# Kernel tuning notes

Measured on AMD Instinct MI355X. Metric: run time of the kernel, lower is better.

Reference implementation:

```python
import jax, jax.numpy as jnp
import numpy as np

LN_EPS = 1e-5

def _layer_norm(x, w, b):
    m = jnp.mean(x, axis=-1, keepdims=True)
    v = jnp.mean(jnp.square(x - m), axis=-1, keepdims=True)
    return (x - m) * jax.lax.rsqrt(v + LN_EPS) * w + b

def setup_inputs() -> dict:
    key = jax.random.key(0)
    ks = jax.random.split(key, 6)
    B, T, D, H = 64, 512, 512, 512
    x = jax.random.normal(ks[0], (B, T, D), dtype=jnp.float32)
    h = jax.random.normal(ks[1], (B, H), dtype=jnp.float32)
    # orthogonal-ish init approximated by scaled normal (math-equivalent shapes)
    w_ih = jax.random.normal(ks[2], (3 * H, D), dtype=jnp.float32) / np.sqrt(D)
    b_ih = jnp.zeros((3 * H,), dtype=jnp.float32)
    w_hh = jax.random.normal(ks[3], (3 * H, H), dtype=jnp.float32) / np.sqrt(H)
    b_hh = jnp.zeros((3 * H,), dtype=jnp.float32)
    ln_r_w = jnp.ones((H,), jnp.float32); ln_r_b = jnp.zeros((H,), jnp.float32)
    ln_z_w = jnp.ones((H,), jnp.float32); ln_z_b = jnp.zeros((H,), jnp.float32)
    ln_n_w = jnp.ones((H,), jnp.float32); ln_n_b = jnp.zeros((H,), jnp.float32)
    return dict(x=x, h=h, w_ih=w_ih, b_ih=b_ih, w_hh=w_hh, b_hh=b_hh,
                ln_r_w=ln_r_w, ln_r_b=ln_r_b, ln_z_w=ln_z_w, ln_z_b=ln_z_b,
                ln_n_w=ln_n_w, ln_n_b=ln_n_b)

def reference(x, h, w_ih, b_ih, w_hh, b_hh, ln_r_w, ln_r_b, ln_z_w, ln_z_b, ln_n_w, ln_n_b):
    H = h.shape[-1]
    # precompute input gate projections for all timesteps: [B, T, 3H] -> [T, B, 3H]
    x_gates_all = jnp.einsum('btd,gd->btg', x, w_ih) + b_ih
    x_gates_all = jnp.swapaxes(x_gates_all, 0, 1)

    def step(h, x_gates):
        h_gates = jnp.matmul(h, w_hh.T) + b_hh
        x_r, x_z, x_n = jnp.split(x_gates, 3, axis=-1)
        h_r, h_z, h_n = jnp.split(h_gates, 3, axis=-1)
        r = jax.nn.sigmoid(_layer_norm(x_r + h_r, ln_r_w, ln_r_b))
        z = jax.nn.sigmoid(_layer_norm(x_z + h_z, ln_z_w, ln_z_b))
        n = jnp.tanh(_layer_norm(x_n + r * h_n, ln_n_w, ln_n_b))
        h_new = (1.0 - z) * n + z * h
        return h_new, h_new

    h_last, out_tbh = jax.lax.scan(step, h, x_gates_all)
    out = jnp.swapaxes(out_tbh, 0, 1)  # [B, T, H]
    return out, h_last
```

## Files before the change

### kernel.cpp

```cpp
#include <hip/hip_runtime.h>
#include <hip/hip_bf16.h>

#define B_ 64
#define T_ 512
#define D_ 512
#define H_ 512
#define G3 1536
#define NBLK 16

typedef float f32x4 __attribute__((ext_vector_type(4)));
typedef __bf16 bf16x8 __attribute__((ext_vector_type(8)));

#define LDSP 56
#define WPITCH 520

union bfpack { bf16x8 v; __hip_bfloat16 h[8]; };

__device__ inline bf16x8 cvt8(const float* __restrict__ p) {
    float4 f0 = *(const float4*)p;
    float4 f1 = *(const float4*)(p + 4);
    bfpack u;
    u.h[0] = __float2bfloat16(f0.x); u.h[1] = __float2bfloat16(f0.y);
    u.h[2] = __float2bfloat16(f0.z); u.h[3] = __float2bfloat16(f0.w);
    u.h[4] = __float2bfloat16(f1.x); u.h[5] = __float2bfloat16(f1.y);
    u.h[6] = __float2bfloat16(f1.z); u.h[7] = __float2bfloat16(f1.w);
    return u.v;
}

__global__ void k0_init(const float* __restrict__ h_in,
                        __hip_bfloat16* __restrict__ hb,
                        unsigned int* __restrict__ ctr) {
    int i = blockIdx.x * blockDim.x + threadIdx.x;
    if (i < B_ * H_) hb[i] = __float2bfloat16(h_in[i]);
    if (i < 1024)    ctr[i] = 0u;
}

__global__ __launch_bounds__(256) void k1_xgemm(
    const float* __restrict__ X, const float* __restrict__ W,
    const float* __restrict__ bias, __hip_bfloat16* __restrict__ XG)
{
    __shared__ __align__(16) __hip_bfloat16 la[128 * LDSP];
    __shared__ __align__(16) __hip_bfloat16 lb[128 * LDSP];
    int tid = threadIdx.x, bx = blockIdx.x;
    int m0 = (bx / 12) * 128, n0 = (bx % 12) * 128;
    int wave = tid >> 6, lane = tid & 63;
    int wh = wave >> 1, ww = wave & 1;
    int l15 = lane & 15, kq = lane >> 4;

    f32x4 acc[4][4];
    #pragma unroll
    for (int i = 0; i < 4; i++)
        #pragma unroll
        for (int j = 0; j < 4; j++) acc[i][j] = (f32x4){0.f, 0.f, 0.f, 0.f};

    for (int kt = 0; kt < 16; ++kt) {
        int k0 = kt * 32;
        for (int s = tid; s < 512; s += 256) {
            int r = s >> 2, c = s & 3;
            *(bf16x8*)&la[r * LDSP + c * 8] = cvt8(&X[(size_t)(m0 + r) * D_ + k0 + c * 8]);
            *(bf16x8*)&lb[r * LDSP + c * 8] = cvt8(&W[(size_t)(n0 + r) * D_ + k0 + c * 8]);
        }
        __syncthreads();
        bf16x8 af[4], bq[4];
        #pragma unroll
        for (int i = 0; i < 4; i++)
            af[i] = *(const bf16x8*)&la[(wh * 64 + i * 16 + l15) * LDSP + kq * 8];
        #pragma unroll
        for (int j = 0; j < 4; j++)
            bq[j] = *(const bf16x8*)&lb[(ww * 64 + j * 16 + l15) * LDSP + kq * 8];
        #pragma unroll
        for (int i = 0; i < 4; i++)
            #pragma unroll
            for (int j = 0; j < 4; j++)
                acc[i][j] = __builtin_amdgcn_mfma_f32_16x16x32_bf16(af[i], bq[j], acc[i][j], 0, 0, 0);
        __syncthreads();
    }
    #pragma unroll
    for (int i = 0; i < 4; i++)
        #pragma unroll
        for (int j = 0; j < 4; j++)
            #pragma unroll
            for (int r = 0; r < 4; r++) {
                int m = m0 + wh * 64 + i * 16 + kq * 4 + r;
                int n = n0 + ww * 64 + j * 16 + l15;
                int b = m >> 9, t = m & 511;
                XG[((size_t)t * B_ + b) * G3 + n] = __float2bfloat16(acc[i][j][r] + bias[n]);
            }
}

__global__ __launch_bounds__(512, 1) void k2_recur(
    const float* __restrict__ h_in, const float* __restrict__ Whh,
    const float* __restrict__ b_hh,
    const float* __restrict__ lnrw, const float* __restrict__ lnrb,
    const float* __restrict__ lnzw, const float* __restrict__ lnzb,
    const float* __restrict__ lnnw, const float* __restrict__ lnnb,
    const __hip_bfloat16* __restrict__ XG,
    float* __restrict__ HG, __hip_bfloat16* __restrict__ HB,
    unsigned int* __restrict__ ctr, float* __restrict__ out)
{
    __shared__ __align__(16) __hip_bfloat16 lw[96 * WPITCH];
    __shared__ float sc[32];

    const int tid = threadIdx.x;
    const int blk = blockIdx.x;
    const int n0 = blk * 96;
    const int s0 = blk * 4;

    for (int idx = tid; idx < 96 * 64; idx += 512) {
        int row = idx >> 6, ch = idx & 63;
        *(bf16x8*)&lw[row * WPITCH + ch * 8] = cvt8(&Whh[(size_t)(n0 + row) * H_ + ch * 8]);
    }

    const int w = tid >> 6, lane = tid & 63;
    const int l15 = lane & 15, kq = lane >> 4;
    const int mt = w >> 1;
    const int nj0 = (w & 1) * 3;

    const int sid = tid >> 7;
    const int c = tid & 127;
    const int b = s0 + sid;

    float bhr[4], bhz[4], bhn[4], wr[4], br_[4], wz[4], bz_[4], wn[4], bn_[4], hf[4];
    #pragma unroll
    for (int j = 0; j < 4; j++) {
        int col = c + j * 128;
        bhr[j] = b_hh[col];       bhz[j] = b_hh[512 + col]; bhn[j] = b_hh[1024 + col];
        wr[j] = lnrw[col]; br_[j] = lnrb[col];
        wz[j] = lnzw[col]; bz_[j] = lnzb[col];
        wn[j] = lnnw[col]; bn_[j] = lnnb[col];
        hf[j] = h_in[b * H_ + col];
    }
    __syncthreads();

    const float inv = 1.0f / 512.0f;

    for (int t = 0; t < T_; ++t) {
        bf16x8 afr[16];
        {
            const __hip_bfloat16* hrow = HB + (mt * 16 + l15) * H_ + kq * 8;
            #pragma unroll
            for (int kt = 0; kt < 16; kt++) afr[kt] = *(const bf16x8*)(hrow + kt * 32);
        }
        f32x4 a0 = {0,0,0,0}, a1 = {0,0,0,0}, a2 = {0,0,0,0};
        #pragma unroll
        for (int kt = 0; kt < 16; kt++) {
            bf16x8 b0 = *(const bf16x8*)&lw[((nj0    ) * 16 + l15) * WPITCH + kt * 32 + kq * 8];
            bf16x8 b1 = *(const bf16x8*)&lw[((nj0 + 1) * 16 + l15) * WPITCH + kt * 32 + kq * 8];
            bf16x8 b2 = *(const bf16x8*)&lw[((nj0 + 2) * 16 + l15) * WPITCH + kt * 32 + kq * 8];
            a0 = __builtin_amdgcn_mfma_f32_16x16x32_bf16(afr[kt], b0, a0, 0, 0, 0);
            a1 = __builtin_amdgcn_mfma_f32_16x16x32_bf16(afr[kt], b1, a1, 0, 0, 0);
            a2 = __builtin_amdgcn_mfma_f32_16x16x32_bf16(afr[kt], b2, a2, 0, 0, 0);
        }
        {
            int rowb = mt * 16 + kq * 4;
            int colb = n0 + nj0 * 16 + l15;
            #pragma unroll
            for (int r = 0; r < 4; r++) {
                HG[(rowb + r) * G3 + colb     ] = a0[r];
                HG[(rowb + r) * G3 + colb + 16] = a1[r];
                HG[(rowb + r) * G3 + colb + 32] = a2[r];
            }
        }
        __syncthreads();
        if (tid == 0) {
            __threadfence();
            __hip_atomic_fetch_add(&ctr[2 * t], 1u, __ATOMIC_RELEASE, __HIP_MEMORY_SCOPE_AGENT);
            while (__hip_atomic_load(&ctr[2 * t], __ATOMIC_ACQUIRE, __HIP_MEMORY_SCOPE_AGENT) < NBLK) {}
            __threadfence();
        }
        __syncthreads();

        const float* hgrow = HG + (size_t)b * G3;
        const __hip_bfloat16* xgrow = XG + ((size_t)t * B_ + b) * G3;
        float ar[4], az[4], hgn[4], xn[4];
        float sr = 0.f, ssr = 0.f, sz = 0.f, ssz = 0.f;
        #pragma unroll
        for (int j = 0; j < 4; j++) {
            int col = c + j * 128;
            float hr = hgrow[col] + bhr[j];
            float hz = hgrow[512 + col] + bhz[j];
            hgn[j] = hgrow[1024 + col] + bhn[j];
            ar[j] = __bfloat162float(xgrow[col]) + hr;
            az[j] = __bfloat162float(xgrow[512 + col]) + hz;
            xn[j] = __bfloat162float(xgrow[1024 + col]);
            sr += ar[j]; ssr += ar[j] * ar[j];
            sz += az[j]; ssz += az[j] * az[j];
        }
        #pragma unroll
        for (int off = 32; off; off >>= 1) {
            sr += __shfl_down(sr, off); ssr += __shfl_down(ssr, off);
            sz += __shfl_down(sz, off); ssz += __shfl_down(ssz, off);
        }
        if (lane == 0) { sc[w * 4] = sr; sc[w * 4 + 1] = ssr; sc[w * 4 + 2] = sz; sc[w * 4 + 3] = ssz; }
        __syncthreads();
        {
            int w0 = sid * 2;
            sr  = sc[w0 * 4]     + sc[(w0 + 1) * 4];
            ssr = sc[w0 * 4 + 1] + sc[(w0 + 1) * 4 + 1];
            sz  = sc[w0 * 4 + 2] + sc[(w0 + 1) * 4 + 2];
            ssz = sc[w0 * 4 + 3] + sc[(w0 + 1) * 4 + 3];
        }
        __syncthreads();
        float mr = sr * inv, vr = ssr * inv - mr * mr, rstd_r = rsqrtf(vr + 1e-5f);
        float mz = sz * inv, vz = ssz * inv - mz * mz, rstd_z = rsqrtf(vz + 1e-5f);
        float rg[4], zg[4], an[4];
        float sn = 0.f, ssn = 0.f;
        #pragma unroll
        for (int j = 0; j < 4; j++) {
            rg[j] = 1.f / (1.f + __expf(-((ar[j] - mr) * rstd_r * wr[j] + br_[j])));
            zg[j] = 1.f / (1.f + __expf(-((az[j] - mz) * rstd_z * wz[j] + bz_[j])));
            an[j] = xn[j] + rg[j] * hgn[j];
            sn += an[j]; ssn += an[j] * an[j];
        }
        #pragma unroll
        for (int off = 32; off; off >>= 1) {
            sn += __shfl_down(sn, off); ssn += __shfl_down(ssn, off);
        }
        if (lane == 0) { sc[w * 4] = sn; sc[w * 4 + 1] = ssn; }
        __syncthreads();
        {
            int w0 = sid * 2;
            sn  = sc[w0 * 4]     + sc[(w0 + 1) * 4];
            ssn = sc[w0 * 4 + 1] + sc[(w0 + 1) * 4 + 1];
        }
        __syncthreads();
        float mn = sn * inv, vn = ssn * inv - mn * mn, rstd_n = rsqrtf(vn + 1e-5f);
        float hnew[4];
        #pragma unroll
        for (int j = 0; j < 4; j++) {
            float ng = tanhf((an[j] - mn) * rstd_n * wn[j] + bn_[j]);
            hnew[j] = (1.f - zg[j]) * ng + zg[j] * hf[j];
            hf[j] = hnew[j];
            HB[b * H_ + c + j * 128] = __float2bfloat16(hnew[j]);
        }
        __syncthreads();
        if (tid == 0) {
            __threadfence();
            __hip_atomic_fetch_add(&ctr[2 * t + 1], 1u, __ATOMIC_RELEASE, __HIP_MEMORY_SCOPE_AGENT);
            while (__hip_atomic_load(&ctr[2 * t + 1], __ATOMIC_ACQUIRE, __HIP_MEMORY_SCOPE_AGENT) < NBLK) {}
            __threadfence();
        }
        __syncthreads();
        #pragma unroll
        for (int j = 0; j < 4; j++)
            out[((size_t)b * T_ + t) * H_ + c + j * 128] = hnew[j];
        if (t == T_ - 1) {
            #pragma unroll
            for (int j = 0; j < 4; j++)
                out[(size_t)B_ * T_ * H_ + b * H_ + c + j * 128] = hnew[j];
        }
    }
}

extern "C" void kernel_launch(void* const* d_in, const int* in_sizes, int n_in,
                              void* d_out, int out_size, void* d_ws, size_t ws_size,
                              hipStream_t stream)
{
    const float* x    = (const float*)d_in[0];
    const float* h    = (const float*)d_in[1];
    const float* w_ih = (const float*)d_in[2];
    const float* b_ih = (const float*)d_in[3];
    const float* w_hh = (const float*)d_in[4];
    const float* b_hh = (const float*)d_in[5];
    const float* lnrw = (const float*)d_in[6];
    const float* lnrb = (const float*)d_in[7];
    const float* lnzw = (const float*)d_in[8];
    const float* lnzb = (const float*)d_in[9];
    const float* lnnw = (const float*)d_in[10];
    const float* lnnb = (const float*)d_in[11];
    float* out = (float*)d_out;

    char* ws = (char*)d_ws;
    __hip_bfloat16* XG = (__hip_bfloat16*)ws;
    float*          HG = (float*)(ws + 100663296);
    __hip_bfloat16* HB = (__hip_bfloat16*)(ws + 101056512);
    unsigned int*  CTR = (unsigned int*)(ws + 101122048);

    k0_init<<<128, 256, 0, stream>>>(h, HB, CTR);
    k1_xgemm<<<3072, 256, 0, stream>>>(x, w_ih, b_ih, XG);
    k2_recur<<<NBLK, 512, 0, stream>>>(h, w_hh, b_hh,
        lnrw, lnrb, lnzw, lnzb, lnnw, lnnb, XG, HG, HB, CTR, out);
}
```

Baseline: 5.619 ms.

## Use relaxed coherent atomics for grid barrier and vectorize per-thread column layout

Replaces the release/acquire fenced grid barriers with relaxed atomic counters. Cross-block data (HG, HB) is now written and read through relaxed agent-scope atomic loads and stores, with an explicit vmcnt wait before each barrier. Each thread now owns four contiguous columns instead of strided ones, so the XG, HG, HB and output accesses become vectorized 64-bit or 128-bit operations, and the XG load is issued before the recurrent matmul. The aim is to cut fence and cache-flush cost on each of the 1024 barriers, but this relies on relaxed ordering plus waitcnt to keep visibility correct, which is risky.

```diff
diff --git a/kernel.cpp b/kernel.cpp
--- a/kernel.cpp
+++ b/kernel.cpp
@@ -10,11 +10,15 @@
 
 typedef float f32x4 __attribute__((ext_vector_type(4)));
 typedef __bf16 bf16x8 __attribute__((ext_vector_type(8)));
+typedef unsigned long long qword;
 
 #define LDSP 56
 #define WPITCH 520
 
 union bfpack { bf16x8 v; __hip_bfloat16 h[8]; };
+union q2bf { qword q[2]; bf16x8 v; };
+union qf2  { qword q; float f[2]; };
+union qbf4 { qword q; __hip_bfloat16 h[4]; };
 
 __device__ inline bf16x8 cvt8(const float* __restrict__ p) {
     float4 f0 = *(const float4*)p;
@@ -25,6 +29,24 @@
     u.h[4] = __float2bfloat16(f1.x); u.h[5] = __float2bfloat16(f1.y);
     u.h[6] = __float2bfloat16(f1.z); u.h[7] = __float2bfloat16(f1.w);
     return u.v;
+}
+
+__device__ inline qword ld_coh(const qword* p) {
+    return __hip_atomic_load(p, __ATOMIC_RELAXED, __HIP_MEMORY_SCOPE_AGENT);
+}
+__device__ inline void st_coh(float* p, float v) {
+    __hip_atomic_store(p, v, __ATOMIC_RELAXED, __HIP_MEMORY_SCOPE_AGENT);
+}
+__device__ inline void st_coh64(qword* p, qword v) {
+    __hip_atomic_store(p, v, __ATOMIC_RELAXED, __HIP_MEMORY_SCOPE_AGENT);
+}
+
+__device__ inline void barrier_slot(unsigned int* ctr, int slot) {
+    __hip_atomic_fetch_add(&ctr[slot], 1u, __ATOMIC_RELAXED, __HIP_MEMORY_SCOPE_AGENT);
+    int spins = 0;
+    while (__hip_atomic_load(&ctr[slot], __ATOMIC_RELAXED, __HIP_MEMORY_SCOPE_AGENT) < NBLK) {
+        if (++spins > (1 << 22)) { spins = 0; __threadfence(); }
+    }
 }
 
 __global__ void k0_init(const float* __restrict__ h_in,
@@ -123,7 +145,7 @@
     float bhr[4], bhz[4], bhn[4], wr[4], br_[4], wz[4], bz_[4], wn[4], bn_[4], hf[4];
     #pragma unroll
     for (int j = 0; j < 4; j++) {
-        int col = c + j * 128;
+        int col = 4 * c + j;
         bhr[j] = b_hh[col];       bhz[j] = b_hh[512 + col]; bhn[j] = b_hh[1024 + col];
         wr[j] = lnrw[col]; br_[j] = lnrb[col];
         wz[j] = lnzw[col]; bz_[j] = lnzb[col];
@@ -133,13 +155,21 @@
     __syncthreads();
 
     const float inv = 1.0f / 512.0f;
+    const qword* hbq_base = (const qword*)HB + (size_t)(mt * 16 + l15) * 128 + kq * 2;
+    const float* hg_mine = HG + (size_t)b * G3 + 4 * c;
 
     for (int t = 0; t < T_; ++t) {
-        bf16x8 afr[16];
-        {
-            const __hip_bfloat16* hrow = HB + (mt * 16 + l15) * H_ + kq * 8;
-            #pragma unroll
-            for (int kt = 0; kt < 16; kt++) afr[kt] = *(const bf16x8*)(hrow + kt * 32);
+        const qword* xgq = (const qword*)(XG + ((size_t)t * B_ + b) * G3) + c;
+        qbf4 xr8, xz8, xn8;
+        xr8.q = xgq[0];
+        xz8.q = xgq[128];
+        xn8.q = xgq[256];
+
+        q2bf afr[16];
+        #pragma unroll
+        for (int kt = 0; kt < 16; kt++) {
+            afr[kt].q[0] = ld_coh(hbq_base + kt * 8);
+            afr[kt].q[1] = ld_coh(hbq_base + kt * 8 + 1);
         }
         f32x4 a0 = {0,0,0,0}, a1 = {0,0,0,0}, a2 = {0,0,0,0};
         #pragma unroll
@@ -147,42 +177,44 @@
             bf16x8 b0 = *(const bf16x8*)&lw[((nj0    ) * 16 + l15) * WPITCH + kt * 32 + kq * 8];
             bf16x8 b1 = *(const bf16x8*)&lw[((nj0 + 1) * 16 + l15) * WPITCH + kt * 32 + kq * 8];
             bf16x8 b2 = *(const bf16x8*)&lw[((nj0 + 2) * 16 + l15) * WPITCH + kt * 32 + kq * 8];
-            a0 = __builtin_amdgcn_mfma_f32_16x16x32_bf16(afr[kt], b0, a0, 0, 0, 0);
-            a1 = __builtin_amdgcn_mfma_f32_16x16x32_bf16(afr[kt], b1, a1, 0, 0, 0);
-            a2 = __builtin_amdgcn_mfma_f32_16x16x32_bf16(afr[kt], b2, a2, 0, 0, 0);
+            a0 = __builtin_amdgcn_mfma_f32_16x16x32_bf16(afr[kt].v, b0, a0, 0, 0, 0);
+            a1 = __builtin_amdgcn_mfma_f32_16x16x32_bf16(afr[kt].v, b1, a1, 0, 0, 0);
+            a2 = __builtin_amdgcn_mfma_f32_16x16x32_bf16(afr[kt].v, b2, a2, 0, 0, 0);
         }
         {
             int rowb = mt * 16 + kq * 4;
             int colb = n0 + nj0 * 16 + l15;
             #pragma unroll
             for (int r = 0; r < 4; r++) {
-                HG[(rowb + r) * G3 + colb     ] = a0[r];
-                HG[(rowb + r) * G3 + colb + 16] = a1[r];
-                HG[(rowb + r) * G3 + colb + 32] = a2[r];
+                st_coh(&HG[(rowb + r) * G3 + colb     ], a0[r]);
+                st_coh(&HG[(rowb + r) * G3 + colb + 16], a1[r]);
+                st_coh(&HG[(rowb + r) * G3 + colb + 32], a2[r]);
             }
         }
-        __syncthreads();
-        if (tid == 0) {
-            __threadfence();
-            __hip_atomic_fetch_add(&ctr[2 * t], 1u, __ATOMIC_RELEASE, __HIP_MEMORY_SCOPE_AGENT);
-            while (__hip_atomic_load(&ctr[2 * t], __ATOMIC_ACQUIRE, __HIP_MEMORY_SCOPE_AGENT) < NBLK) {}
-            __threadfence();
-        }
-        __syncthreads();
-
-        const float* hgrow = HG + (size_t)b * G3;
-        const __hip_bfloat16* xgrow = XG + ((size_t)t * B_ + b) * G3;
+        asm volatile("s_waitcnt vmcnt(0)" ::: "memory");
+        __syncthreads();
+        if (tid == 0) barrier_slot(ctr, 2 * t);
+        __syncthreads();
+
+        qf2 hr01, hr23, hz01, hz23, hn01, hn23;
+        hr01.q = ld_coh((const qword*)(hg_mine));
+        hr23.q = ld_coh((const qword*)(hg_mine + 2));
+        hz01.q = ld_coh((const qword*)(hg_mine + 512));
+        hz23.q = ld_coh((const qword*)(hg_mine + 514));
+        hn01.q = ld_coh((const qword*)(hg_mine + 1024));
+        hn23.q = ld_coh((const qword*)(hg_mine + 1026));
+        float hgr[4]  = {hr01.f[0], hr01.f[1], hr23.f[0], hr23.f[1]};
+        float hgz[4]  = {hz01.f[0], hz01.f[1], hz23.f[0], hz23.f[1]};
+        float hgnv[4] = {hn01.f[0], hn01.f[1], hn23.f[0], hn23.f[1]};
+
         float ar[4], az[4], hgn[4], xn[4];
         float sr = 0.f, ssr = 0.f, sz = 0.f, ssz = 0.f;
         #pragma unroll
         for (int j = 0; j < 4; j++) {
-            int col = c + j * 128;
-            float hr = hgrow[col] + bhr[j];
-            float hz = hgrow[512 + col] + bhz[j];
-            hgn[j] = hgrow[1024 + col] + bhn[j];
-            ar[j] = __bfloat162float(xgrow[col]) + hr;
-            az[j] = __bfloat162float(xgrow[512 + col]) + hz;
-            xn[j] = __bfloat162float(xgrow[1024 + col]);
+            ar[j]  = __bfloat162float(xr8.h[j]) + hgr[j] + bhr[j];
+            az[j]  = __bfloat162float(xz8.h[j]) + hgz[j] + bhz[j];
+            hgn[j] = hgnv[j] + bhn[j];
+            xn[j]  = __bfloat162float(xn8.h[j]);
             sr += ar[j]; ssr += ar[j] * ar[j];
             sz += az[j]; ssz += az[j] * az[j];
         }
@@ -226,28 +258,24 @@
         __syncthreads();
         float mn = sn * inv, vn = ssn * inv - mn * mn, rstd_n = rsqrtf(vn + 1e-5f);
         float hnew[4];
+        qbf4 hbnew;
         #pragma unroll
         for (int j = 0; j < 4; j++) {
             float ng = tanhf((an[j] - mn) * rstd_n * wn[j] + bn_[j]);
             hnew[j] = (1.f - zg[j]) * ng + zg[j] * hf[j];
             hf[j] = hnew[j];
-            HB[b * H_ + c + j * 128] = __float2bfloat16(hnew[j]);
-        }
-        __syncthreads();
-        if (tid == 0) {
-            __threadfence();
-            __hip_atomic_fetch_add(&ctr[2 * t + 1], 1u, __ATOMIC_RELEASE, __HIP_MEMORY_SCOPE_AGENT);
-            while (__hip_atomic_load(&ctr[2 * t + 1], __ATOMIC_ACQUIRE, __HIP_MEMORY_SCOPE_AGENT) < NBLK) {}
-            __threadfence();
-        }
-        __syncthreads();
-        #pragma unroll
-        for (int j = 0; j < 4; j++)
-            out[((size_t)b * T_ + t) * H_ + c + j * 128] = hnew[j];
+            hbnew.h[j] = __float2bfloat16(hnew[j]);
+        }
+        st_coh64((qword*)HB + (size_t)b * 128 + c, hbnew.q);
+        asm volatile("s_waitcnt vmcnt(0)" ::: "memory");
+        __syncthreads();
+        if (tid == 0) barrier_slot(ctr, 2 * t + 1);
+        __syncthreads();
+        *(f32x4*)(out + ((size_t)b * T_ + t) * H_ + 4 * c) =
+            (f32x4){hnew[0], hnew[1], hnew[2], hnew[3]};
         if (t == T_ - 1) {
-            #pragma unroll
-            for (int j = 0; j < 4; j++)
-                out[(size_t)B_ * T_ * H_ + b * H_ + c + j * 128] = hnew[j];
+            *(f32x4*)(out + (size_t)B_ * T_ * H_ + b * H_ + 4 * c) =
+                (f32x4){hnew[0], hnew[1], hnew[2], hnew[3]};
         }
     }
 }
```

Measured after the change: 6.931 ms. +23.4%, slower.
